# Kernel tuning notes

Measured on AMD Instinct MI355X. Metric: run time of the kernel, lower is better.

The kernel has to match this reference:

```python
import jax, jax.numpy as jnp
import numpy as np
import itertools

K = 3            # kernel size
KSS = K * K      # kernel_space_size = 9
STRIDE = 1
PAD = 1
ORDERS = (1, 2)


def _unfold(x, k, stride, pad):
    """torch.nn.Unfold equivalent: [B,C,H,W] -> [B, C*k*k, L], feature order (c, kh, kw)."""
    B, C, H, W = x.shape
    xp = jnp.pad(x, ((0, 0), (0, 0), (pad, pad), (pad, pad)))
    oh = (H + 2 * pad - k) // stride + 1
    ow = (W + 2 * pad - k) // stride + 1
    rows = (jnp.arange(oh) * stride)[:, None] + jnp.arange(k)[None, :]  # [oh,k]
    cols = (jnp.arange(ow) * stride)[:, None] + jnp.arange(k)[None, :]  # [ow,k]
    # broadcast indices -> patches [B,C,oh,ow,k,k]
    p = xp[:, :, rows[:, None, :, None], cols[None, :, None, :]]
    p = p.transpose(0, 1, 4, 5, 2, 3).reshape(B, C * k * k, oh * ow)
    return p, oh, ow


def _superdiag_keep(kss, order):
    """Complement of VolterraKernel2d mask: True at sorted-combination positions."""
    keep = np.zeros((kss,) * order, dtype=bool)
    for idx in itertools.combinations_with_replacement(range(kss), order):
        keep[idx] = True
    return keep.reshape(-1)


def _volterra_features(xp4, order):
    """xp4: [B,C,L,kss] -> masked+scaled order-`order` features [B,C,L,kss**order]."""
    if order == 1:
        return xp4  # masking/scaling disabled for order 1 in the original
    f = xp4
    for _ in range(order - 1):
        f = jnp.einsum('bclp,bclq->bclpq', f, xp4)
        f = f.reshape(*f.shape[:3], -1)
    keep = _superdiag_keep(KSS, order)                 # static numpy bool
    scale = 1.0 / np.sqrt(keep.sum())                   # 1/sqrt(#kept) == original scaling_factor
    return f * jnp.asarray(keep, f.dtype) * jnp.asarray(scale, f.dtype)


def setup_inputs() -> dict:
    key = jax.random.key(0)
    k1, k2, k3 = jax.random.split(key, 3)
    B, C, H, W = 4, 64, 64, 64
    out_ch = 64
    x = jax.random.normal(k1, (B, C, H, W), dtype=jnp.float32)
    W1 = jax.random.normal(k2, (C * KSS, out_ch), dtype=jnp.float32) * 0.05
    W2 = jax.random.normal(k3, (C * KSS ** 2, out_ch), dtype=jnp.float32) * 0.02
    bias_w = jnp.zeros((out_ch, 1, 1), dtype=jnp.float32)
    return {"x": x, "W1": W1, "W2": W2, "bias_w": bias_w}


def reference(x, W1, W2, bias_w):
    B, C, H, W = x.shape
    unf, oh, ow = _unfold(x, K, STRIDE, PAD)           # [B, C*kss, L]
    L = oh * ow
    xp4 = unf.reshape(B, C, KSS, L).transpose(0, 1, 3, 2)  # [B,C,L,kss]
    out = 0.0
    for order, Wt in zip(ORDERS, (W1, W2)):
        f = _volterra_features(xp4, order)             # [B,C,L,kss**order]
        feat = f.transpose(0, 2, 1, 3).reshape(B, L, -1)   # [B,L,C*kss**order]
        out = out + feat @ Wt                          # [B,L,out_ch]
    out_ch = W1.shape[1]
    # faithful to the original: raw view of [B,L,out_ch] memory into [B,out_ch,oh,ow]
    out = out.reshape(B, out_ch, oh, ow) + bias_w
    return out
```

## Files before the change

### kernel.cpp

```cpp
#include <hip/hip_runtime.h>
#include <hip/hip_bf16.h>


typedef __bf16 bf16x8 __attribute__((ext_vector_type(8)));
typedef float f32x16 __attribute__((ext_vector_type(16)));

#define SCALE_Q 0.14907119849998599f

__device__ __constant__ int g_pairP[45] = {
  0,0,0,0,0,0,0,0,0, 1,1,1,1,1,1,1,1, 2,2,2,2,2,2,2,
  3,3,3,3,3,3, 4,4,4,4,4, 5,5,5,5, 6,6,6, 7,7, 8};
__device__ __constant__ int g_pairQ[45] = {
  0,1,2,3,4,5,6,7,8, 1,2,3,4,5,6,7,8, 2,3,4,5,6,7,8,
  3,4,5,6,7,8, 4,5,6,7,8, 5,6,7,8, 6,7,8, 7,8, 8};

union AFrag { unsigned int u[4]; bf16x8 v; };
union BFrag { uint4 q; bf16x8 v; };

__device__ inline unsigned int pack_bf16x2(float a, float b){
  union { __hip_bfloat16 h; unsigned short s; } ca, cb;
  ca.h = __float2bfloat16(a);
  cb.h = __float2bfloat16(b);
  return (unsigned int)ca.s | ((unsigned int)cb.s << 16);
}

__device__ inline void half_swap(unsigned int U, unsigned int V,
                                 unsigned int& o0, unsigned int& o1, int lane){
#if __has_builtin(__builtin_amdgcn_permlane32_swap)
  auto rr = __builtin_amdgcn_permlane32_swap(U, V, false, false);
  o0 = rr[0]; o1 = rr[1];
#else
  unsigned int Ux = (unsigned int)__shfl_xor((int)U, 32);
  unsigned int Vx = (unsigned int)__shfl_xor((int)V, 32);
  const bool hi = (lane >= 32);
  o0 = hi ? Vx : U;
  o1 = hi ? V : Ux;
#endif
}

__global__ __launch_bounds__(256) void volt_pack(const float* __restrict__ W1,
                                                 const float* __restrict__ W2,
                                                 __hip_bfloat16* __restrict__ Bpack){
  int g = blockIdx.x * 256 + threadIdx.x;
  int c     = g >> 9;
  int inner = g & 511;
  int lane  = inner & 63;
  int ks    = inner >> 7;
  int nb    = (inner >> 6) & 1;
  int n     = nb * 32 + (lane & 31);
  int kh    = lane >> 5;
  #pragma unroll
  for (int j = 0; j < 8; ++j){
    int f = ks * 16 + kh * 8 + j;
    float wv = 0.0f;
    if (f < 9)       wv = W1[(c * 9 + f) * 64 + n];
    else if (f < 54){
      int t = f - 9;
      wv = SCALE_Q * W2[(c * 81 + g_pairP[t] * 9 + g_pairQ[t]) * 64 + n];
    }
    Bpack[(size_t)g * 8 + j] = __float2bfloat16(wv);
  }
}

__global__ __launch_bounds__(512, 2) void volt_main(const float* __restrict__ x,
                                                    const uint4* __restrict__ Bpack,
                                                    const float* __restrict__ bias_w,
                                                    float* __restrict__ out){
  __shared__ float red[8 * 4096];
  const int tid  = threadIdx.x;
  const int lane = tid & 63;
  const int kv   = tid >> 6;
  const int b    = blockIdx.x >> 6;
  const int h0   = blockIdx.x & 63;

  const int hm = (h0 > 0)  ? h0 - 1 : 0;
  const int hp = (h0 < 63) ? h0 + 1 : 63;
  const float* xw   = x + ((size_t)(b * 64 + kv * 8)) * 4096;
  const uint4* bsrc = Bpack + (size_t)(kv * 8) * 512 + lane;

  constexpr int kP[45] = {
    0,0,0,0,0,0,0,0,0, 1,1,1,1,1,1,1,1, 2,2,2,2,2,2,2,
    3,3,3,3,3,3, 4,4,4,4,4, 5,5,5,5, 6,6,6, 7,7, 8};
  constexpr int kQ[45] = {
    0,1,2,3,4,5,6,7,8, 1,2,3,4,5,6,7,8, 2,3,4,5,6,7,8,
    3,4,5,6,7,8, 4,5,6,7,8, 5,6,7,8, 6,7,8, 7,8, 8};

  f32x16 acc00{}, acc01{}, acc10{}, acc11{};

  auto loadB = [&](int i, BFrag (&B)[8]){
    const uint4* s = bsrc + (size_t)i * 512;
    #pragma unroll
    for (int j = 0; j < 8; ++j) B[j].q = s[j * 64];
  };
  auto loadX = [&](int i, float (&v)[3]){
    const float* xc = xw + (size_t)i * 4096;
    v[0] = xc[hm * 64 + lane];
    v[1] = xc[h0 * 64 + lane];
    v[2] = xc[hp * 64 + lane];
  };

  auto compute = [&](const float (&cx)[3], const BFrag (&Bf)[8]){
    float xp[9];
    #pragma unroll
    for (int dh = 0; dh < 3; ++dh){
      float mid = cx[dh];
      if (dh == 0 && h0 == 0)  mid = 0.f;
      if (dh == 2 && h0 == 63) mid = 0.f;
      float lf = __shfl(mid, lane - 1);
      float rt = __shfl(mid, lane + 1);
      xp[dh * 3 + 0] = (lane == 0)  ? 0.f : lf;
      xp[dh * 3 + 1] = mid;
      xp[dh * 3 + 2] = (lane == 63) ? 0.f : rt;
    }
    float pr[45];
    #pragma unroll
    for (int t = 0; t < 45; ++t) pr[t] = xp[kP[t]] * xp[kQ[t]];

    unsigned int d[32];
    #pragma unroll
    for (int s = 0; s < 32; ++s){
      const int f0 = 2 * s, f1 = 2 * s + 1;
      float a  = (f0 < 9) ? xp[f0] : ((f0 < 54) ? pr[f0 - 9] : 0.0f);
      float b2 = (f1 < 9) ? xp[f1] : ((f1 < 54) ? pr[f1 - 9] : 0.0f);
      d[s] = pack_bf16x2(a, b2);
    }

    AFrag a0[4], a1[4];
    #pragma unroll
    for (int ks = 0; ks < 4; ++ks){
      #pragma unroll
      for (int j = 0; j < 4; ++j){
        half_swap(d[ks * 8 + j], d[ks * 8 + 4 + j], a0[ks].u[j], a1[ks].u[j], lane);
      }
    }

    __builtin_amdgcn_s_setprio(1);
    #pragma unroll
    for (int ks = 0; ks < 4; ++ks){
      acc00 = __builtin_amdgcn_mfma_f32_32x32x16_bf16(a0[ks].v, Bf[ks*2+0].v, acc00, 0, 0, 0);
      acc01 = __builtin_amdgcn_mfma_f32_32x32x16_bf16(a0[ks].v, Bf[ks*2+1].v, acc01, 0, 0, 0);
      acc10 = __builtin_amdgcn_mfma_f32_32x32x16_bf16(a1[ks].v, Bf[ks*2+0].v, acc10, 0, 0, 0);
      acc11 = __builtin_amdgcn_mfma_f32_32x32x16_bf16(a1[ks].v, Bf[ks*2+1].v, acc11, 0, 0, 0);
    }
    __builtin_amdgcn_s_setprio(0);
  };

  BFrag bufA[8], bufB[8];
  float cxA[3], cxB[3];
  loadB(0, bufA); loadX(0, cxA);

  #pragma unroll 1
  for (int ii = 0; ii < 4; ++ii){
    const int i0 = ii * 2;
    loadB(i0 + 1, bufB); loadX(i0 + 1, cxB);
    compute(cxA, bufA);
    if (ii < 3){ loadB(i0 + 2, bufA); loadX(i0 + 2, cxA); }
    compute(cxB, bufB);
  }

  {
    const int colbase = lane & 31;
    const int rowadd  = 4 * (lane >> 5);
    #pragma unroll
    for (int r = 0; r < 16; ++r){
      int rl = (r & 3) + 8 * (r >> 2) + rowadd;
      red[kv * 4096 + (rl)      * 64 + colbase     ] = acc00[r];
      red[kv * 4096 + (rl)      * 64 + colbase + 32] = acc01[r];
      red[kv * 4096 + (rl + 32) * 64 + colbase     ] = acc10[r];
      red[kv * 4096 + (rl + 32) * 64 + colbase + 32] = acc11[r];
    }
  }
  __syncthreads();
  const float bias = bias_w[h0];
  float* outp = out + (size_t)b * 262144 + (size_t)h0 * 4096;
  #pragma unroll
  for (int j = 0; j < 8; ++j){
    int oidx = j * 512 + tid;
    float v = bias;
    #pragma unroll
    for (int kvv = 0; kvv < 8; ++kvv) v += red[kvv * 4096 + oidx];
    outp[oidx] = v;
  }
}

extern "C" void kernel_launch(void* const* d_in, const int* in_sizes, int n_in,
                              void* d_out, int out_size, void* d_ws, size_t ws_size,
                              hipStream_t stream){
  const float* x      = (const float*)d_in[0];
  const float* W1     = (const float*)d_in[1];
  const float* W2     = (const float*)d_in[2];
  const float* bias_w = (const float*)d_in[3];
  float* out = (float*)d_out;
  __hip_bfloat16* Bpack = (__hip_bfloat16*)d_ws;

  volt_pack<<<128, 256, 0, stream>>>(W1, W2, Bpack);
  volt_main<<<256, 512, 0, stream>>>(x, (const uint4*)d_ws, bias_w, out);
}
```

Baseline: 24.26 us.

## Fuse weight packing into main kernel, reading fp32 weights directly

Drops the separate weight-pack kernel launch. Each wave of the main kernel now loads the fp32 W1/W2 rows it needs (selected by the symmetric pair tables), converts them to bf16 in registers, and moves the quadratic scale onto the x values. The explicit double-buffered load pipeline is replaced by a fully unrolled loop over channels. In exchange, every block re-reads and re-converts the scattered fp32 weights (256 blocks instead of one pack pass), using more load bandwidth and registers, and it relies on the compiler to overlap those loads with compute.

```diff
diff --git a/kernel.cpp b/kernel.cpp
--- a/kernel.cpp
+++ b/kernel.cpp
@@ -7,15 +7,15 @@
 
 #define SCALE_Q 0.14907119849998599f
 
-__device__ __constant__ int g_pairP[45] = {
+constexpr int cP[45] = {
   0,0,0,0,0,0,0,0,0, 1,1,1,1,1,1,1,1, 2,2,2,2,2,2,2,
   3,3,3,3,3,3, 4,4,4,4,4, 5,5,5,5, 6,6,6, 7,7, 8};
-__device__ __constant__ int g_pairQ[45] = {
+constexpr int cQ[45] = {
   0,1,2,3,4,5,6,7,8, 1,2,3,4,5,6,7,8, 2,3,4,5,6,7,8,
   3,4,5,6,7,8, 4,5,6,7,8, 5,6,7,8, 6,7,8, 7,8, 8};
 
 union AFrag { unsigned int u[4]; bf16x8 v; };
-union BFrag { uint4 q; bf16x8 v; };
+union BFrag { unsigned int u[4]; bf16x8 v; };
 
 __device__ inline unsigned int pack_bf16x2(float a, float b){
   union { __hip_bfloat16 h; unsigned short s; } ca, cb;
@@ -38,32 +38,35 @@
 #endif
 }
 
-__global__ __launch_bounds__(256) void volt_pack(const float* __restrict__ W1,
-                                                 const float* __restrict__ W2,
-                                                 __hip_bfloat16* __restrict__ Bpack){
-  int g = blockIdx.x * 256 + threadIdx.x;
-  int c     = g >> 9;
-  int inner = g & 511;
-  int lane  = inner & 63;
-  int ks    = inner >> 7;
-  int nb    = (inner >> 6) & 1;
-  int n     = nb * 32 + (lane & 31);
-  int kh    = lane >> 5;
+template<int KH>
+__device__ inline void loadW(const float* __restrict__ W1, const float* __restrict__ W2,
+                             int c, int col, float (&rw)[64]){
   #pragma unroll
-  for (int j = 0; j < 8; ++j){
-    int f = ks * 16 + kh * 8 + j;
-    float wv = 0.0f;
-    if (f < 9)       wv = W1[(c * 9 + f) * 64 + n];
-    else if (f < 54){
-      int t = f - 9;
-      wv = SCALE_Q * W2[(c * 81 + g_pairP[t] * 9 + g_pairQ[t]) * 64 + n];
+  for (int ks = 0; ks < 4; ++ks){
+    #pragma unroll
+    for (int j = 0; j < 4; ++j){
+      #pragma unroll
+      for (int h = 0; h < 2; ++h){
+        const int F = ks * 16 + KH * 8 + 2 * j + h;
+        float v0, v1;
+        if (F < 9){
+          v0 = W1[(c * 9 + F) * 64 + col];
+          v1 = W1[(c * 9 + F) * 64 + col + 32];
+        } else if (F < 54){
+          const int row = c * 81 + cP[F - 9] * 9 + cQ[F - 9];
+          v0 = W2[row * 64 + col];
+          v1 = W2[row * 64 + col + 32];
+        } else { v0 = 0.0f; v1 = 0.0f; }
+        rw[ks * 16 + j * 4 + h]     = v0;
+        rw[ks * 16 + j * 4 + 2 + h] = v1;
+      }
     }
-    Bpack[(size_t)g * 8 + j] = __float2bfloat16(wv);
   }
 }
 
 __global__ __launch_bounds__(512, 2) void volt_main(const float* __restrict__ x,
-                                                    const uint4* __restrict__ Bpack,
+                                                    const float* __restrict__ W1,
+                                                    const float* __restrict__ W2,
                                                     const float* __restrict__ bias_w,
                                                     float* __restrict__ out){
   __shared__ float red[8 * 4096];
@@ -73,56 +76,64 @@
   const int b    = blockIdx.x >> 6;
   const int h0   = blockIdx.x & 63;
 
+  const int kh   = lane >> 5;
+  const int colb = lane & 31;
+
   const int hm = (h0 > 0)  ? h0 - 1 : 0;
   const int hp = (h0 < 63) ? h0 + 1 : 63;
-  const float* xw   = x + ((size_t)(b * 64 + kv * 8)) * 4096;
-  const uint4* bsrc = Bpack + (size_t)(kv * 8) * 512 + lane;
-
-  constexpr int kP[45] = {
-    0,0,0,0,0,0,0,0,0, 1,1,1,1,1,1,1,1, 2,2,2,2,2,2,2,
-    3,3,3,3,3,3, 4,4,4,4,4, 5,5,5,5, 6,6,6, 7,7, 8};
-  constexpr int kQ[45] = {
-    0,1,2,3,4,5,6,7,8, 1,2,3,4,5,6,7,8, 2,3,4,5,6,7,8,
-    3,4,5,6,7,8, 4,5,6,7,8, 5,6,7,8, 6,7,8, 7,8, 8};
+  const float* xw = x + ((size_t)(b * 64 + kv * 8)) * 4096;
 
   f32x16 acc00{}, acc01{}, acc10{}, acc11{};
 
-  auto loadB = [&](int i, BFrag (&B)[8]){
-    const uint4* s = bsrc + (size_t)i * 512;
+  #pragma unroll
+  for (int i = 0; i < 8; ++i){
+    const int c = kv * 8 + i;
+
+    float rw[64];
+    if (kh == 0) loadW<0>(W1, W2, c, colb, rw);
+    else         loadW<1>(W1, W2, c, colb, rw);
+
+    const float* xc = xw + (size_t)i * 4096;
+    float cx0 = xc[hm * 64 + lane];
+    float cx1 = xc[h0 * 64 + lane];
+    float cx2 = xc[hp * 64 + lane];
+
+    float xp[9];
+    {
+      float rows[3] = {cx0, cx1, cx2};
+      #pragma unroll
+      for (int dh = 0; dh < 3; ++dh){
+        float mid = rows[dh];
+        if (dh == 0 && h0 == 0)  mid = 0.f;
+        if (dh == 2 && h0 == 63) mid = 0.f;
+        float lf = __shfl(mid, lane - 1);
+        float rt = __shfl(mid, lane + 1);
+        xp[dh * 3 + 0] = (lane == 0)  ? 0.f : lf;
+        xp[dh * 3 + 1] = mid;
+        xp[dh * 3 + 2] = (lane == 63) ? 0.f : rt;
+      }
+    }
+    float xq[9];
     #pragma unroll
-    for (int j = 0; j < 8; ++j) B[j].q = s[j * 64];
-  };
-  auto loadX = [&](int i, float (&v)[3]){
-    const float* xc = xw + (size_t)i * 4096;
-    v[0] = xc[hm * 64 + lane];
-    v[1] = xc[h0 * 64 + lane];
-    v[2] = xc[hp * 64 + lane];
-  };
-
-  auto compute = [&](const float (&cx)[3], const BFrag (&Bf)[8]){
-    float xp[9];
-    #pragma unroll
-    for (int dh = 0; dh < 3; ++dh){
-      float mid = cx[dh];
-      if (dh == 0 && h0 == 0)  mid = 0.f;
-      if (dh == 2 && h0 == 63) mid = 0.f;
-      float lf = __shfl(mid, lane - 1);
-      float rt = __shfl(mid, lane + 1);
-      xp[dh * 3 + 0] = (lane == 0)  ? 0.f : lf;
-      xp[dh * 3 + 1] = mid;
-      xp[dh * 3 + 2] = (lane == 63) ? 0.f : rt;
-    }
-    float pr[45];
-    #pragma unroll
-    for (int t = 0; t < 45; ++t) pr[t] = xp[kP[t]] * xp[kQ[t]];
+    for (int j = 0; j < 9; ++j) xq[j] = xp[j] * SCALE_Q;
 
     unsigned int d[32];
     #pragma unroll
     for (int s = 0; s < 32; ++s){
       const int f0 = 2 * s, f1 = 2 * s + 1;
-      float a  = (f0 < 9) ? xp[f0] : ((f0 < 54) ? pr[f0 - 9] : 0.0f);
-      float b2 = (f1 < 9) ? xp[f1] : ((f1 < 54) ? pr[f1 - 9] : 0.0f);
+      float a  = (f0 < 9) ? xp[f0] : ((f0 < 54) ? xq[cP[f0-9]] * xp[cQ[f0-9]] : 0.0f);
+      float b2 = (f1 < 9) ? xp[f1] : ((f1 < 54) ? xq[cP[f1-9]] * xp[cQ[f1-9]] : 0.0f);
       d[s] = pack_bf16x2(a, b2);
+    }
+
+    BFrag Bf[8];
+    #pragma unroll
+    for (int ks = 0; ks < 4; ++ks){
+      #pragma unroll
+      for (int j = 0; j < 4; ++j){
+        Bf[ks*2+0].u[j] = pack_bf16x2(rw[ks*16 + j*4 + 0], rw[ks*16 + j*4 + 1]);
+        Bf[ks*2+1].u[j] = pack_bf16x2(rw[ks*16 + j*4 + 2], rw[ks*16 + j*4 + 3]);
+      }
     }
 
     AFrag a0[4], a1[4];
@@ -143,31 +154,17 @@
       acc11 = __builtin_amdgcn_mfma_f32_32x32x16_bf16(a1[ks].v, Bf[ks*2+1].v, acc11, 0, 0, 0);
     }
     __builtin_amdgcn_s_setprio(0);
-  };
-
-  BFrag bufA[8], bufB[8];
-  float cxA[3], cxB[3];
-  loadB(0, bufA); loadX(0, cxA);
-
-  #pragma unroll 1
-  for (int ii = 0; ii < 4; ++ii){
-    const int i0 = ii * 2;
-    loadB(i0 + 1, bufB); loadX(i0 + 1, cxB);
-    compute(cxA, bufA);
-    if (ii < 3){ loadB(i0 + 2, bufA); loadX(i0 + 2, cxA); }
-    compute(cxB, bufB);
   }
 
   {
-    const int colbase = lane & 31;
-    const int rowadd  = 4 * (lane >> 5);
+    const int rowadd = 4 * kh;
     #pragma unroll
     for (int r = 0; r < 16; ++r){
       int rl = (r & 3) + 8 * (r >> 2) + rowadd;
-      red[kv * 4096 + (rl)      * 64 + colbase     ] = acc00[r];
-      red[kv * 4096 + (rl)      * 64 + colbase + 32] = acc01[r];
-      red[kv * 4096 + (rl + 32) * 64 + colbase     ] = acc10[r];
-      red[kv * 4096 + (rl + 32) * 64 + colbase + 32] = acc11[r];
+      red[kv * 4096 + (rl)      * 64 + colb     ] = acc00[r];
+      red[kv * 4096 + (rl)      * 64 + colb + 32] = acc01[r];
+      red[kv * 4096 + (rl + 32) * 64 + colb     ] = acc10[r];
+      red[kv * 4096 + (rl + 32) * 64 + colb + 32] = acc11[r];
     }
   }
   __syncthreads();
@@ -191,8 +188,7 @@
   const float* W2     = (const float*)d_in[2];
   const float* bias_w = (const float*)d_in[3];
   float* out = (float*)d_out;
-  __hip_bfloat16* Bpack = (__hip_bfloat16*)d_ws;
+  (void)d_ws; (void)ws_size;
 
-  volt_pack<<<128, 256, 0, stream>>>(W1, W2, Bpack);
-  volt_main<<<256, 512, 0, stream>>>(x, (const uint4*)d_ws, bias_w, out);
+  volt_main<<<256, 512, 0, stream>>>(x, W1, W2, bias_w, out);
 }
```

After: 26.58 us. 9.6% more time.

## Stage weight and input loads through LDS with async global_load_lds double buffering

Applied to the files above, without the earlier changes.

Replaces the register-held B-fragment and x loads with asynchronous global-to-LDS copies into a per-wave double buffer, synchronised with explicit vmcnt waits. The halo neighbours are now read from LDS instead of being taken with cross-lane shuffles. A-fragment packing is restructured per k-step to shorten register live ranges. The goal is to lower VGPR pressure and overlap memory latency with MFMA work. The cost is a much larger LDS footprint (144KB), which may limit occupancy to one block per CU, plus extra LDS reads.

```diff
diff --git a/kernel.cpp b/kernel.cpp
--- a/kernel.cpp
+++ b/kernel.cpp
@@ -15,7 +15,6 @@
   3,4,5,6,7,8, 4,5,6,7,8, 5,6,7,8, 6,7,8, 7,8, 8};
 
 union AFrag { unsigned int u[4]; bf16x8 v; };
-union BFrag { uint4 q; bf16x8 v; };
 
 __device__ inline unsigned int pack_bf16x2(float a, float b){
   union { __hip_bfloat16 h; unsigned short s; } ca, cb;
@@ -37,6 +36,15 @@
   o1 = hi ? V : Ux;
 #endif
 }
+
+#define WAIT_VM(N) \
+  do { asm volatile("s_waitcnt vmcnt(" #N ")" ::: "memory"); \
+       __builtin_amdgcn_sched_barrier(0); } while (0)
+
+#define GL2LDS(gsrc, ldst, SZ) \
+  __builtin_amdgcn_global_load_lds( \
+    (const __attribute__((address_space(1))) void*)(const void*)(gsrc), \
+    (__attribute__((address_space(3))) void*)(void*)(ldst), SZ, 0, 0)
 
 __global__ __launch_bounds__(256) void volt_pack(const float* __restrict__ W1,
                                                  const float* __restrict__ W2,
@@ -66,7 +74,7 @@
                                                     const uint4* __restrict__ Bpack,
                                                     const float* __restrict__ bias_w,
                                                     float* __restrict__ out){
-  __shared__ float red[8 * 4096];
+  __shared__ alignas(16) char smem[147456];
   const int tid  = threadIdx.x;
   const int lane = tid & 63;
   const int kv   = tid >> 6;
@@ -77,6 +85,7 @@
   const int hp = (h0 < 63) ? h0 + 1 : 63;
   const float* xw   = x + ((size_t)(b * 64 + kv * 8)) * 4096;
   const uint4* bsrc = Bpack + (size_t)(kv * 8) * 512 + lane;
+  char* mylds = smem + kv * 18432;
 
   constexpr int kP[45] = {
     0,0,0,0,0,0,0,0,0, 1,1,1,1,1,1,1,1, 2,2,2,2,2,2,2,
@@ -87,77 +96,88 @@
 
   f32x16 acc00{}, acc01{}, acc10{}, acc11{};
 
-  auto loadB = [&](int i, BFrag (&B)[8]){
-    const uint4* s = bsrc + (size_t)i * 512;
-    #pragma unroll
-    for (int j = 0; j < 8; ++j) B[j].q = s[j * 64];
+  auto issueCh = [&](int ch, int buf){
+    const uint4* s = bsrc + (size_t)ch * 512;
+    char* db = mylds + buf * 9216;
+    #pragma unroll
+    for (int j = 0; j < 8; ++j) GL2LDS(s + j * 64, db + j * 1024, 16);
+    const float* xc = xw + (size_t)ch * 4096;
+    char* xb = db + 8192;
+    GL2LDS(xc + hm * 64 + lane, xb + 0,   4);
+    GL2LDS(xc + h0 * 64 + lane, xb + 256, 4);
+    GL2LDS(xc + hp * 64 + lane, xb + 512, 4);
   };
-  auto loadX = [&](int i, float (&v)[3]){
-    const float* xc = xw + (size_t)i * 4096;
-    v[0] = xc[hm * 64 + lane];
-    v[1] = xc[h0 * 64 + lane];
-    v[2] = xc[hp * 64 + lane];
-  };
-
-  auto compute = [&](const float (&cx)[3], const BFrag (&Bf)[8]){
+
+  auto compute = [&](int buf){
+    const char*  db = mylds + buf * 9216;
+    const float* xb = reinterpret_cast<const float*>(db + 8192);
+    const int lm = (lane == 0)  ? 0  : lane - 1;
+    const int lp = (lane == 63) ? 63 : lane + 1;
+
     float xp[9];
     #pragma unroll
     for (int dh = 0; dh < 3; ++dh){
-      float mid = cx[dh];
-      if (dh == 0 && h0 == 0)  mid = 0.f;
-      if (dh == 2 && h0 == 63) mid = 0.f;
-      float lf = __shfl(mid, lane - 1);
-      float rt = __shfl(mid, lane + 1);
-      xp[dh * 3 + 0] = (lane == 0)  ? 0.f : lf;
-      xp[dh * 3 + 1] = mid;
-      xp[dh * 3 + 2] = (lane == 63) ? 0.f : rt;
+      float vL = xb[dh * 64 + lm];
+      float vM = xb[dh * 64 + lane];
+      float vR = xb[dh * 64 + lp];
+      if (dh == 0 && h0 == 0)  { vL = 0.f; vM = 0.f; vR = 0.f; }
+      if (dh == 2 && h0 == 63) { vL = 0.f; vM = 0.f; vR = 0.f; }
+      xp[dh * 3 + 0] = (lane == 0)  ? 0.f : vL;
+      xp[dh * 3 + 1] = vM;
+      xp[dh * 3 + 2] = (lane == 63) ? 0.f : vR;
     }
     float pr[45];
     #pragma unroll
     for (int t = 0; t < 45; ++t) pr[t] = xp[kP[t]] * xp[kQ[t]];
 
-    unsigned int d[32];
-    #pragma unroll
-    for (int s = 0; s < 32; ++s){
-      const int f0 = 2 * s, f1 = 2 * s + 1;
-      float a  = (f0 < 9) ? xp[f0] : ((f0 < 54) ? pr[f0 - 9] : 0.0f);
-      float b2 = (f1 < 9) ? xp[f1] : ((f1 < 54) ? pr[f1 - 9] : 0.0f);
-      d[s] = pack_bf16x2(a, b2);
-    }
-
     AFrag a0[4], a1[4];
     #pragma unroll
     for (int ks = 0; ks < 4; ++ks){
+      unsigned int dl[8];
+      #pragma unroll
+      for (int e = 0; e < 8; ++e){
+        const int f0 = ks * 16 + 2 * e, f1 = f0 + 1;
+        float va = (f0 < 9) ? xp[f0] : ((f0 < 54) ? pr[f0 - 9] : 0.0f);
+        float vb = (f1 < 9) ? xp[f1] : ((f1 < 54) ? pr[f1 - 9] : 0.0f);
+        dl[e] = pack_bf16x2(va, vb);
+      }
       #pragma unroll
       for (int j = 0; j < 4; ++j){
-        half_swap(d[ks * 8 + j], d[ks * 8 + 4 + j], a0[ks].u[j], a1[ks].u[j], lane);
+        half_swap(dl[j], dl[4 + j], a0[ks].u[j], a1[ks].u[j], lane);
       }
     }
 
     __builtin_amdgcn_s_setprio(1);
     #pragma unroll
     for (int ks = 0; ks < 4; ++ks){
-      acc00 = __builtin_amdgcn_mfma_f32_32x32x16_bf16(a0[ks].v, Bf[ks*2+0].v, acc00, 0, 0, 0);
-      acc01 = __builtin_amdgcn_mfma_f32_32x32x16_bf16(a0[ks].v, Bf[ks*2+1].v, acc01, 0, 0, 0);
-      acc10 = __builtin_amdgcn_mfma_f32_32x32x16_bf16(a1[ks].v, Bf[ks*2+0].v, acc10, 0, 0, 0);
-      acc11 = __builtin_amdgcn_mfma_f32_32x32x16_bf16(a1[ks].v, Bf[ks*2+1].v, acc11, 0, 0, 0);
+      bf16x8 b0 = *reinterpret_cast<const bf16x8*>(db + ((ks * 2 + 0) * 64 + lane) * 16);
+      bf16x8 b1 = *reinterpret_cast<const bf16x8*>(db + ((ks * 2 + 1) * 64 + lane) * 16);
+      acc00 = __builtin_amdgcn_mfma_f32_32x32x16_bf16(a0[ks].v, b0, acc00, 0, 0, 0);
+      acc01 = __builtin_amdgcn_mfma_f32_32x32x16_bf16(a0[ks].v, b1, acc01, 0, 0, 0);
+      acc10 = __builtin_amdgcn_mfma_f32_32x32x16_bf16(a1[ks].v, b0, acc10, 0, 0, 0);
+      acc11 = __builtin_amdgcn_mfma_f32_32x32x16_bf16(a1[ks].v, b1, acc11, 0, 0, 0);
     }
     __builtin_amdgcn_s_setprio(0);
   };
 
-  BFrag bufA[8], bufB[8];
-  float cxA[3], cxB[3];
-  loadB(0, bufA); loadX(0, cxA);
-
+  issueCh(0, 0);
   #pragma unroll 1
-  for (int ii = 0; ii < 4; ++ii){
-    const int i0 = ii * 2;
-    loadB(i0 + 1, bufB); loadX(i0 + 1, cxB);
-    compute(cxA, bufA);
-    if (ii < 3){ loadB(i0 + 2, bufA); loadX(i0 + 2, cxA); }
-    compute(cxB, bufB);
-  }
-
+  for (int ii = 0; ii < 3; ++ii){
+    issueCh(2 * ii + 1, 1);
+    WAIT_VM(11);
+    compute(0);
+    issueCh(2 * ii + 2, 0);
+    WAIT_VM(11);
+    compute(1);
+  }
+  issueCh(7, 1);
+  WAIT_VM(11);
+  compute(0);
+  WAIT_VM(0);
+  compute(1);
+
+  __syncthreads();
+  float* red = reinterpret_cast<float*>(smem);
   {
     const int colbase = lane & 31;
     const int rowadd  = 4 * (lane >> 5);
```

Measured after the change: 25.27 us. 4.1% more time.

## Split channel reduction across 16 waves with staged LDS accumulate

Applied to the files above, without the earlier changes.

Doubles the block to 1024 threads so each wave handles 4 input channels instead of 8. Features are computed per k-step inside a fully unrolled loop, which lowers register pressure, and the explicit double-buffered prefetch is dropped. The cross-wave reduction becomes two phases: the upper 8 waves store their partials to LDS, then the lower 8 add theirs in place. This trades per-wave latency hiding for more waves per block, and adds a sync plus read-modify-write LDS traffic.

```diff
diff --git a/kernel.cpp b/kernel.cpp
--- a/kernel.cpp
+++ b/kernel.cpp
@@ -11,6 +11,13 @@
   0,0,0,0,0,0,0,0,0, 1,1,1,1,1,1,1,1, 2,2,2,2,2,2,2,
   3,3,3,3,3,3, 4,4,4,4,4, 5,5,5,5, 6,6,6, 7,7, 8};
 __device__ __constant__ int g_pairQ[45] = {
+  0,1,2,3,4,5,6,7,8, 1,2,3,4,5,6,7,8, 2,3,4,5,6,7,8,
+  3,4,5,6,7,8, 4,5,6,7,8, 5,6,7,8, 6,7,8, 7,8, 8};
+
+constexpr int cP[45] = {
+  0,0,0,0,0,0,0,0,0, 1,1,1,1,1,1,1,1, 2,2,2,2,2,2,2,
+  3,3,3,3,3,3, 4,4,4,4,4, 5,5,5,5, 6,6,6, 7,7, 8};
+constexpr int cQ[45] = {
   0,1,2,3,4,5,6,7,8, 1,2,3,4,5,6,7,8, 2,3,4,5,6,7,8,
   3,4,5,6,7,8, 4,5,6,7,8, 5,6,7,8, 6,7,8, 7,8, 8};
 
@@ -38,6 +45,12 @@
 #endif
 }
 
+__device__ inline float slotv(int F, const float (&xp)[9]){
+  if (F < 9)  return xp[F];
+  if (F < 54) return xp[cP[F - 9]] * xp[cQ[F - 9]];
+  return 0.0f;
+}
+
 __global__ __launch_bounds__(256) void volt_pack(const float* __restrict__ W1,
                                                  const float* __restrict__ W2,
                                                  __hip_bfloat16* __restrict__ Bpack){
@@ -62,10 +75,10 @@
   }
 }
 
-__global__ __launch_bounds__(512, 2) void volt_main(const float* __restrict__ x,
-                                                    const uint4* __restrict__ Bpack,
-                                                    const float* __restrict__ bias_w,
-                                                    float* __restrict__ out){
+__global__ __launch_bounds__(1024, 4) void volt_main(const float* __restrict__ x,
+                                                     const uint4* __restrict__ Bpack,
+                                                     const float* __restrict__ bias_w,
+                                                     float* __restrict__ out){
   __shared__ float red[8 * 4096];
   const int tid  = threadIdx.x;
   const int lane = tid & 63;
@@ -75,107 +88,94 @@
 
   const int hm = (h0 > 0)  ? h0 - 1 : 0;
   const int hp = (h0 < 63) ? h0 + 1 : 63;
-  const float* xw   = x + ((size_t)(b * 64 + kv * 8)) * 4096;
-  const uint4* bsrc = Bpack + (size_t)(kv * 8) * 512 + lane;
-
-  constexpr int kP[45] = {
-    0,0,0,0,0,0,0,0,0, 1,1,1,1,1,1,1,1, 2,2,2,2,2,2,2,
-    3,3,3,3,3,3, 4,4,4,4,4, 5,5,5,5, 6,6,6, 7,7, 8};
-  constexpr int kQ[45] = {
-    0,1,2,3,4,5,6,7,8, 1,2,3,4,5,6,7,8, 2,3,4,5,6,7,8,
-    3,4,5,6,7,8, 4,5,6,7,8, 5,6,7,8, 6,7,8, 7,8, 8};
+  const float* xw   = x + ((size_t)(b * 64 + kv * 4)) * 4096;
+  const uint4* bsrc = Bpack + (size_t)(kv * 4) * 512 + lane;
 
   f32x16 acc00{}, acc01{}, acc10{}, acc11{};
 
-  auto loadB = [&](int i, BFrag (&B)[8]){
-    const uint4* s = bsrc + (size_t)i * 512;
-    #pragma unroll
-    for (int j = 0; j < 8; ++j) B[j].q = s[j * 64];
-  };
-  auto loadX = [&](int i, float (&v)[3]){
+  #pragma unroll
+  for (int i = 0; i < 4; ++i){
     const float* xc = xw + (size_t)i * 4096;
-    v[0] = xc[hm * 64 + lane];
-    v[1] = xc[h0 * 64 + lane];
-    v[2] = xc[hp * 64 + lane];
-  };
+    float cx0 = xc[hm * 64 + lane];
+    float cx1 = xc[h0 * 64 + lane];
+    float cx2 = xc[hp * 64 + lane];
 
-  auto compute = [&](const float (&cx)[3], const BFrag (&Bf)[8]){
     float xp[9];
-    #pragma unroll
-    for (int dh = 0; dh < 3; ++dh){
-      float mid = cx[dh];
-      if (dh == 0 && h0 == 0)  mid = 0.f;
-      if (dh == 2 && h0 == 63) mid = 0.f;
-      float lf = __shfl(mid, lane - 1);
-      float rt = __shfl(mid, lane + 1);
-      xp[dh * 3 + 0] = (lane == 0)  ? 0.f : lf;
-      xp[dh * 3 + 1] = mid;
-      xp[dh * 3 + 2] = (lane == 63) ? 0.f : rt;
-    }
-    float pr[45];
-    #pragma unroll
-    for (int t = 0; t < 45; ++t) pr[t] = xp[kP[t]] * xp[kQ[t]];
-
-    unsigned int d[32];
-    #pragma unroll
-    for (int s = 0; s < 32; ++s){
-      const int f0 = 2 * s, f1 = 2 * s + 1;
-      float a  = (f0 < 9) ? xp[f0] : ((f0 < 54) ? pr[f0 - 9] : 0.0f);
-      float b2 = (f1 < 9) ? xp[f1] : ((f1 < 54) ? pr[f1 - 9] : 0.0f);
-      d[s] = pack_bf16x2(a, b2);
-    }
-
-    AFrag a0[4], a1[4];
-    #pragma unroll
-    for (int ks = 0; ks < 4; ++ks){
+    {
+      float rows[3] = {cx0, cx1, cx2};
       #pragma unroll
-      for (int j = 0; j < 4; ++j){
-        half_swap(d[ks * 8 + j], d[ks * 8 + 4 + j], a0[ks].u[j], a1[ks].u[j], lane);
+      for (int dh = 0; dh < 3; ++dh){
+        float mid = rows[dh];
+        if (dh == 0 && h0 == 0)  mid = 0.f;
+        if (dh == 2 && h0 == 63) mid = 0.f;
+        float lf = __shfl(mid, lane - 1);
+        float rt = __shfl(mid, lane + 1);
+        xp[dh * 3 + 0] = (lane == 0)  ? 0.f : lf;
+        xp[dh * 3 + 1] = mid;
+        xp[dh * 3 + 2] = (lane == 63) ? 0.f : rt;
       }
     }
 
-    __builtin_amdgcn_s_setprio(1);
+    const uint4* s = bsrc + (size_t)i * 512;
+
     #pragma unroll
     for (int ks = 0; ks < 4; ++ks){
-      acc00 = __builtin_amdgcn_mfma_f32_32x32x16_bf16(a0[ks].v, Bf[ks*2+0].v, acc00, 0, 0, 0);
-      acc01 = __builtin_amdgcn_mfma_f32_32x32x16_bf16(a0[ks].v, Bf[ks*2+1].v, acc01, 0, 0, 0);
-      acc10 = __builtin_amdgcn_mfma_f32_32x32x16_bf16(a1[ks].v, Bf[ks*2+0].v, acc10, 0, 0, 0);
-      acc11 = __builtin_amdgcn_mfma_f32_32x32x16_bf16(a1[ks].v, Bf[ks*2+1].v, acc11, 0, 0, 0);
+      BFrag B0, B1;
+      B0.q = s[(ks * 2 + 0) * 64];
+      B1.q = s[(ks * 2 + 1) * 64];
+
+      unsigned int dl[8];
+      #pragma unroll
+      for (int e = 0; e < 8; ++e){
+        const int f0 = ks * 16 + 2 * e;
+        dl[e] = pack_bf16x2(slotv(f0, xp), slotv(f0 + 1, xp));
+      }
+      AFrag a0, a1;
+      #pragma unroll
+      for (int j = 0; j < 4; ++j){
+        half_swap(dl[j], dl[4 + j], a0.u[j], a1.u[j], lane);
+      }
+
+      __builtin_amdgcn_s_setprio(1);
+      acc00 = __builtin_amdgcn_mfma_f32_32x32x16_bf16(a0.v, B0.v, acc00, 0, 0, 0);
+      acc01 = __builtin_amdgcn_mfma_f32_32x32x16_bf16(a0.v, B1.v, acc01, 0, 0, 0);
+      acc10 = __builtin_amdgcn_mfma_f32_32x32x16_bf16(a1.v, B0.v, acc10, 0, 0, 0);
+      acc11 = __builtin_amdgcn_mfma_f32_32x32x16_bf16(a1.v, B1.v, acc11, 0, 0, 0);
+      __builtin_amdgcn_s_setprio(0);
     }
-    __builtin_amdgcn_s_setprio(0);
-  };
-
-  BFrag bufA[8], bufB[8];
-  float cxA[3], cxB[3];
-  loadB(0, bufA); loadX(0, cxA);
-
-  #pragma unroll 1
-  for (int ii = 0; ii < 4; ++ii){
-    const int i0 = ii * 2;
-    loadB(i0 + 1, bufB); loadX(i0 + 1, cxB);
-    compute(cxA, bufA);
-    if (ii < 3){ loadB(i0 + 2, bufA); loadX(i0 + 2, cxA); }
-    compute(cxB, bufB);
   }
 
-  {
-    const int colbase = lane & 31;
-    const int rowadd  = 4 * (lane >> 5);
+  const int colbase = lane & 31;
+  const int rowadd  = 4 * (lane >> 5);
+  float* buf = red + (kv & 7) * 4096;
+
+  if (kv >= 8){
     #pragma unroll
     for (int r = 0; r < 16; ++r){
       int rl = (r & 3) + 8 * (r >> 2) + rowadd;
-      red[kv * 4096 + (rl)      * 64 + colbase     ] = acc00[r];
-      red[kv * 4096 + (rl)      * 64 + colbase + 32] = acc01[r];
-      red[kv * 4096 + (rl + 32) * 64 + colbase     ] = acc10[r];
-      red[kv * 4096 + (rl + 32) * 64 + colbase + 32] = acc11[r];
+      buf[(rl)      * 64 + colbase     ] = acc00[r];
+      buf[(rl)      * 64 + colbase + 32] = acc01[r];
+      buf[(rl + 32) * 64 + colbase     ] = acc10[r];
+      buf[(rl + 32) * 64 + colbase + 32] = acc11[r];
+    }
+  }
+  __syncthreads();
+  if (kv < 8){
+    #pragma unroll
+    for (int r = 0; r < 16; ++r){
+      int rl = (r & 3) + 8 * (r >> 2) + rowadd;
+      buf[(rl)      * 64 + colbase     ] += acc00[r];
+      buf[(rl)      * 64 + colbase + 32] += acc01[r];
+      buf[(rl + 32) * 64 + colbase     ] += acc10[r];
+      buf[(rl + 32) * 64 + colbase + 32] += acc11[r];
     }
   }
   __syncthreads();
   const float bias = bias_w[h0];
   float* outp = out + (size_t)b * 262144 + (size_t)h0 * 4096;
   #pragma unroll
-  for (int j = 0; j < 8; ++j){
-    int oidx = j * 512 + tid;
+  for (int j = 0; j < 4; ++j){
+    int oidx = j * 1024 + tid;
     float v = bias;
     #pragma unroll
     for (int kvv = 0; kvv < 8; ++kvv) v += red[kvv * 4096 + oidx];
@@ -194,5 +194,5 @@
   __hip_bfloat16* Bpack = (__hip_bfloat16*)d_ws;
 
   volt_pack<<<128, 256, 0, stream>>>(W1, W2, Bpack);
-  volt_main<<<256, 512, 0, stream>>>(x, (const uint4*)d_ws, bias_w, out);
+  volt_main<<<256, 1024, 0, stream>>>(x, (const uint4*)d_ws, bias_w, out);
 }
```

Measured after the change: 23.79 us. Within noise of the previous version (-1.9%).
